# Kernel optimization log

Measured on AMD Instinct MI355X. Metric: run time of the kernel, lower is better.

The kernel has to match this reference:

```python
import jax, jax.numpy as jnp
import numpy as np

N_NODES = 50000
N_EDGES = 800000
IN_CH = 128
HID = 64
HEADS = 4
OUT_CH = 10
N_GRAPHS = 512
NEG_SLOPE = 0.2


def setup_inputs() -> dict:
    key = jax.random.key(0)
    ks = jax.random.split(key, 16)
    x = jax.random.normal(ks[0], (N_NODES, IN_CH), dtype=jnp.float32)
    edge_index = jax.random.randint(ks[1], (2, N_EDGES), 0, N_NODES, dtype=jnp.int64)
    batch = jnp.sort(jax.random.randint(ks[2], (N_NODES,), 0, N_GRAPHS, dtype=jnp.int64))
    s = 1.0 / np.sqrt(IN_CH)
    W1 = jax.random.uniform(ks[3], (IN_CH, HEADS * HID), jnp.float32, -s, s)
    att_src1 = jax.random.normal(ks[4], (HEADS, HID), jnp.float32) * 0.1
    att_dst1 = jax.random.normal(ks[5], (HEADS, HID), jnp.float32) * 0.1
    b1 = jnp.zeros((HEADS * HID,), jnp.float32)
    s2 = 1.0 / np.sqrt(HEADS * HID)
    W2 = jax.random.uniform(ks[6], (HEADS * HID, HID), jnp.float32, -s2, s2)
    att_src2 = jax.random.normal(ks[7], (1, HID), jnp.float32) * 0.1
    att_dst2 = jax.random.normal(ks[8], (1, HID), jnp.float32) * 0.1
    b2 = jnp.zeros((HID,), jnp.float32)
    s3 = 1.0 / np.sqrt(HID)
    Wl = jax.random.uniform(ks[9], (HID, OUT_CH), jnp.float32, -s3, s3)
    bl = jnp.zeros((OUT_CH,), jnp.float32)
    return dict(x=x, edge_index=edge_index, batch=batch,
                W1=W1, att_src1=att_src1, att_dst1=att_dst1, b1=b1,
                W2=W2, att_src2=att_src2, att_dst2=att_dst2, b2=b2,
                Wl=Wl, bl=bl)


def gat_conv(x, src, dst, W, att_src, att_dst, bias, heads, out_ch, concat):
    """PyG GATConv: gather -> per-edge attention -> segment softmax over dst -> scatter-add."""
    n = x.shape[0]
    h = (x @ W).reshape(n, heads, out_ch)            # [N,H,C]
    a_s = jnp.sum(h * att_src, axis=-1)              # [N,H]
    a_d = jnp.sum(h * att_dst, axis=-1)              # [N,H]
    e = jax.nn.leaky_relu(a_s[src] + a_d[dst], NEG_SLOPE)  # [E,H]
    m = jax.ops.segment_max(e, dst, num_segments=n)  # stable softmax per dst
    alpha = jnp.exp(e - m[dst])
    denom = jax.ops.segment_sum(alpha, dst, num_segments=n)
    alpha = alpha / denom[dst]
    out = jax.ops.segment_sum(h[src] * alpha[:, :, None], dst, num_segments=n)  # [N,H,C]
    if concat:
        out = out.reshape(n, heads * out_ch)
    else:
        out = out.mean(axis=1)
    return out + bias


def reference(x, edge_index, batch, W1, att_src1, att_dst1, b1,
              W2, att_src2, att_dst2, b2, Wl, bl):
    n = x.shape[0]
    # PyG GATConv default add_self_loops=True
    loops = jnp.arange(n, dtype=edge_index.dtype)
    src = jnp.concatenate([edge_index[0], loops])
    dst = jnp.concatenate([edge_index[1], loops])

    h = jax.nn.elu(gat_conv(x, src, dst, W1, att_src1, att_dst1, b1, HEADS, HID, True))
    h = jax.nn.elu(gat_conv(h, src, dst, W2, att_src2, att_dst2, b2, 1, HID, False))

    # global_mean_pool
    sums = jax.ops.segment_sum(h, batch, num_segments=N_GRAPHS)
    cnts = jax.ops.segment_sum(jnp.ones((n,), h.dtype), batch, num_segments=N_GRAPHS)
    pooled = sums / jnp.maximum(cnts, 1.0)[:, None]

    return pooled @ Wl + bl
```

## Files before the change

kernel.cpp:

```cpp
#include <hip/hip_runtime.h>
#include <hip/hip_bf16.h>
#include <math.h>

#define N_NODES 50000
#define N_EDGES 800000
#define IN_CH 128
#define HID 64
#define HEADS 4
#define OUT_CH 10
#define N_GRAPHS 512
#define NEG_SLOPE 0.2f

using short8_t = __attribute__((ext_vector_type(8))) short;
using f32x4 = __attribute__((ext_vector_type(4))) float;

__device__ __forceinline__ float b2f(unsigned short u) {
    return __uint_as_float(((unsigned)u) << 16);
}
__device__ __forceinline__ unsigned short f2b(float f) {
    __hip_bfloat16 b = __float2bfloat16(f);
    return *(unsigned short*)&b;
}
__device__ __forceinline__ short f2bs(float f) {
    __hip_bfloat16 b = __float2bfloat16(f);
    return *(short*)&b;
}
__device__ __forceinline__ float lrelu(float x) { return x > 0.f ? x : NEG_SLOPE * x; }

__global__ void convw_k(const float* __restrict__ W1, const float* __restrict__ W2,
                        unsigned short* __restrict__ Wt1, unsigned short* __restrict__ Wt2) {
    int idx = blockIdx.x * 256 + threadIdx.x;
    if (idx < 256 * 128) {
        int n = idx / 128, k = idx % 128;
        Wt1[idx] = f2b(W1[(size_t)k * 256 + n]);
    }
    int j = idx - 256 * 128;
    if (j >= 0 && j < 64 * 256) {
        int n = j / 256, k = j % 256;
        Wt2[j] = f2b(W2[(size_t)k * 64 + n]);
    }
}

__global__ __launch_bounds__(256) void mfma_gemm1_k(
        const float* __restrict__ X, const unsigned short* __restrict__ Wt,
        unsigned short* __restrict__ Yb,
        const float* __restrict__ asrc, const float* __restrict__ adst,
        float* __restrict__ As, float* __restrict__ Ad, int M) {
    const int lane = threadIdx.x & 63;
    const int w = threadIdx.x >> 6;
    const int r0 = blockIdx.x * 64 + w * 16;
    const int l15 = lane & 15;
    const int rc = min(r0 + l15, M - 1);
    const int kg = (lane >> 4) * 8;

    f32x4 acc[16] = {};
#pragma unroll
    for (int kc = 0; kc < 4; kc++) {
        int k0 = kc * 32 + kg;
        float4 xa = *(const float4*)&X[(size_t)rc * 128 + k0];
        float4 xb = *(const float4*)&X[(size_t)rc * 128 + k0 + 4];
        short8_t af;
        af[0] = f2bs(xa.x); af[1] = f2bs(xa.y); af[2] = f2bs(xa.z); af[3] = f2bs(xa.w);
        af[4] = f2bs(xb.x); af[5] = f2bs(xb.y); af[6] = f2bs(xb.z); af[7] = f2bs(xb.w);
#pragma unroll
        for (int ct = 0; ct < 16; ct++) {
            int col = ct * 16 + l15;
            short8_t bf = *(const short8_t*)&Wt[(size_t)col * 128 + k0];
            acc[ct] = __builtin_amdgcn_mfma_f32_16x16x32_bf16(af, bf, acc[ct], 0, 0, 0);
        }
    }

    const int rbase = r0 + (lane >> 4) * 4;
#pragma unroll
    for (int reg = 0; reg < 4; reg++) {
        int gr = rbase + reg;
        float s0 = 0.f, s1 = 0.f, s2 = 0.f, s3 = 0.f;
        float d0 = 0.f, d1 = 0.f, d2 = 0.f, d3 = 0.f;
#pragma unroll
        for (int cg = 0; cg < 4; cg++) {
            int c = cg * 16 + l15;
            float v0 = acc[0 * 4 + cg][reg], v1 = acc[1 * 4 + cg][reg];
            float v2 = acc[2 * 4 + cg][reg], v3 = acc[3 * 4 + cg][reg];
            s0 += v0 * asrc[0 * 64 + c]; d0 += v0 * adst[0 * 64 + c];
            s1 += v1 * asrc[1 * 64 + c]; d1 += v1 * adst[1 * 64 + c];
            s2 += v2 * asrc[2 * 64 + c]; d2 += v2 * adst[2 * 64 + c];
            s3 += v3 * asrc[3 * 64 + c]; d3 += v3 * adst[3 * 64 + c];
        }
#pragma unroll
        for (int o = 8; o > 0; o >>= 1) {
            s0 += __shfl_xor(s0, o); d0 += __shfl_xor(d0, o);
            s1 += __shfl_xor(s1, o); d1 += __shfl_xor(d1, o);
            s2 += __shfl_xor(s2, o); d2 += __shfl_xor(d2, o);
            s3 += __shfl_xor(s3, o); d3 += __shfl_xor(d3, o);
        }
        if (l15 == 0 && gr < M) {
            *(float4*)&As[gr * 4] = make_float4(s0, s1, s2, s3);
            *(float4*)&Ad[gr * 4] = make_float4(d0, d1, d2, d3);
        }
    }
#pragma unroll
    for (int reg = 0; reg < 4; reg++) {
        int gr = rbase + reg;
        if (gr >= M) continue;
#pragma unroll
        for (int cg = 0; cg < 4; cg++) {
            int c = cg * 16 + l15;
            ushort4 p;
            p.x = f2b(acc[0 * 4 + cg][reg]);
            p.y = f2b(acc[1 * 4 + cg][reg]);
            p.z = f2b(acc[2 * 4 + cg][reg]);
            p.w = f2b(acc[3 * 4 + cg][reg]);
            *(ushort4*)&Yb[(size_t)gr * 256 + c * 4] = p;
        }
    }
}

__global__ __launch_bounds__(256) void mfma_gemm2_k(
        const unsigned short* __restrict__ Xb, const unsigned short* __restrict__ Wt,
        unsigned short* __restrict__ Yb,
        const float* __restrict__ asrc, const float* __restrict__ adst,
        float* __restrict__ As, float* __restrict__ Ad, int M) {
    const int lane = threadIdx.x & 63;
    const int w = threadIdx.x >> 6;
    const int r0 = blockIdx.x * 64 + w * 16;
    const int l15 = lane & 15;
    const int rc = min(r0 + l15, M - 1);
    const int kg = (lane >> 4) * 8;

    f32x4 acc[4] = {};
#pragma unroll
    for (int kc = 0; kc < 8; kc++) {
        int k0 = kc * 32 + kg;
        short8_t af = *(const short8_t*)&Xb[(size_t)rc * 256 + k0];
#pragma unroll
        for (int ct = 0; ct < 4; ct++) {
            int col = ct * 16 + l15;
            short8_t bf = *(const short8_t*)&Wt[(size_t)col * 256 + k0];
            acc[ct] = __builtin_amdgcn_mfma_f32_16x16x32_bf16(af, bf, acc[ct], 0, 0, 0);
        }
    }

    const int rbase = r0 + (lane >> 4) * 4;
#pragma unroll
    for (int reg = 0; reg < 4; reg++) {
        int gr = rbase + reg;
        float sv = 0.f, dv = 0.f;
#pragma unroll
        for (int ct = 0; ct < 4; ct++) {
            int c = ct * 16 + l15;
            float v = acc[ct][reg];
            sv += v * asrc[c];
            dv += v * adst[c];
        }
#pragma unroll
        for (int o = 8; o > 0; o >>= 1) { sv += __shfl_xor(sv, o); dv += __shfl_xor(dv, o); }
        if (l15 == 0 && gr < M) { As[gr] = sv; Ad[gr] = dv; }
        if (gr < M) {
#pragma unroll
            for (int ct = 0; ct < 4; ct++)
                Yb[(size_t)gr * 64 + ct * 16 + l15] = f2b(acc[ct][reg]);
        }
    }
}

__global__ void hist_k(const int* __restrict__ dst, int* __restrict__ deg,
                       int* __restrict__ rank, int etot) {
    int nth = gridDim.x * 256;
    int i0 = blockIdx.x * 256 + threadIdx.x;
    int i1 = i0 + nth, i2 = i0 + 2 * nth, i3 = i0 + 3 * nth;
    bool v0 = i0 < etot, v1 = i1 < etot, v2 = i2 < etot, v3 = i3 < etot;
    int d0 = 0, d1 = 0, d2 = 0, d3 = 0;
    if (v0) d0 = (i0 < N_EDGES) ? dst[i0] : i0 - N_EDGES;
    if (v1) d1 = (i1 < N_EDGES) ? dst[i1] : i1 - N_EDGES;
    if (v2) d2 = (i2 < N_EDGES) ? dst[i2] : i2 - N_EDGES;
    if (v3) d3 = (i3 < N_EDGES) ? dst[i3] : i3 - N_EDGES;
    int r0 = 0, r1 = 0, r2 = 0, r3 = 0;
    if (v0) r0 = atomicAdd(&deg[d0], 1);
    if (v1) r1 = atomicAdd(&deg[d1], 1);
    if (v2) r2 = atomicAdd(&deg[d2], 1);
    if (v3) r3 = atomicAdd(&deg[d3], 1);
    if (v0) rank[i0] = r0;
    if (v1) rank[i1] = r1;
    if (v2) rank[i2] = r2;
    if (v3) rank[i3] = r3;
}

__global__ void cntg_k(const int* __restrict__ batch, float* __restrict__ cntf) {
    int g = blockIdx.x * 256 + threadIdx.x;
    if (g >= N_GRAPHS) return;
    int lo = 0, hi = N_NODES;
    while (lo < hi) { int mid = (lo + hi) >> 1; if (batch[mid] < g) lo = mid + 1; else hi = mid; }
    int lo2 = lo, hi2 = N_NODES;
    while (lo2 < hi2) { int mid = (lo2 + hi2) >> 1; if (batch[mid] < g + 1) lo2 = mid + 1; else hi2 = mid; }
    cntf[g] = (float)(lo2 - lo);
}

__global__ void blksum_k(const int* __restrict__ deg, int* __restrict__ bsum, int n) {
    int t = threadIdx.x;
    int i = blockIdx.x * 256 + t;
    int v = (i < n) ? deg[i] : 0;
#pragma unroll
    for (int o = 32; o > 0; o >>= 1) v += __shfl_xor(v, o);
    __shared__ int wsum[4];
    if ((t & 63) == 0) wsum[t >> 6] = v;
    __syncthreads();
    if (t == 0) bsum[blockIdx.x] = wsum[0] + wsum[1] + wsum[2] + wsum[3];
}

__global__ void scanb_k(int* __restrict__ bsum, int nb) {
    __shared__ int tmp[256];
    int t = threadIdx.x;
    int v = (t < nb) ? bsum[t] : 0;
    tmp[t] = v;
    __syncthreads();
    for (int o = 1; o < 256; o <<= 1) {
        int u = (t >= o) ? tmp[t - o] : 0;
        __syncthreads();
        tmp[t] += u;
        __syncthreads();
    }
    if (t < nb) bsum[t] = tmp[t] - v;
}

__global__ void scanapply_k(const int* __restrict__ deg, const int* __restrict__ bsum,
                            int* __restrict__ rowptr, int n) {
    __shared__ int tmp[256];
    int t = threadIdx.x;
    int i = blockIdx.x * 256 + t;
    int v = (i < n) ? deg[i] : 0;
    tmp[t] = v;
    __syncthreads();
    for (int o = 1; o < 256; o <<= 1) {
        int u = (t >= o) ? tmp[t - o] : 0;
        __syncthreads();
        tmp[t] += u;
        __syncthreads();
    }
    int boff = bsum[blockIdx.x];
    if (i < n) rowptr[i] = boff + tmp[t] - v;
    if (i == n - 1) rowptr[n] = boff + tmp[t];
}

__global__ void scatter_k(const int* __restrict__ src, const int* __restrict__ dst,
                          const int* __restrict__ rowptr, const int* __restrict__ rank,
                          int* __restrict__ csrc, int etot) {
    int i = blockIdx.x * blockDim.x + threadIdx.x;
    if (i >= etot) return;
    int s, d;
    if (i < N_EDGES) { s = src[i]; d = dst[i]; } else { s = d = i - N_EDGES; }
    csrc[rowptr[d] + rank[i]] = s;
}

__global__ void agg1_k(const int* __restrict__ rowptr, const int* __restrict__ csrc,
                       const float* __restrict__ As, const float* __restrict__ Ad,
                       const __hip_bfloat16* __restrict__ Hb,
                       const float* __restrict__ bias,
                       unsigned short* __restrict__ Outb, int nnodes) {
    __shared__ int ssh[4][64];
    __shared__ float4 wsh[4][64];
    int lane = threadIdx.x & 63;
    int w = threadIdx.x >> 6;
    int node = blockIdx.x * 4 + w;
    int beg = rowptr[node], end = rowptr[node + 1];
    int deg = end - beg;
    const unsigned short* hb = (const unsigned short*)Hb;
    float4 bv = *(const float4*)&Ad[node * 4];
    bool fast = (deg <= 64);
    if (fast) {
        bool act = lane < deg;
        int s = act ? csrc[beg + lane] : 0;
        float4 a = *(const float4*)&As[s * 4];
        float e0 = lrelu(a.x + bv.x), e1 = lrelu(a.y + bv.y);
        float e2 = lrelu(a.z + bv.z), e3 = lrelu(a.w + bv.w);
        if (!act) { e0 = e1 = e2 = e3 = -INFINITY; }
        float m0 = e0, m1 = e1, m2 = e2, m3 = e3;
#pragma unroll
        for (int o = 32; o > 0; o >>= 1) {
            m0 = fmaxf(m0, __shfl_xor(m0, o)); m1 = fmaxf(m1, __shfl_xor(m1, o));
            m2 = fmaxf(m2, __shfl_xor(m2, o)); m3 = fmaxf(m3, __shfl_xor(m3, o));
        }
        float x0 = act ? __expf(e0 - m0) : 0.f;
        float x1 = act ? __expf(e1 - m1) : 0.f;
        float x2 = act ? __expf(e2 - m2) : 0.f;
        float x3 = act ? __expf(e3 - m3) : 0.f;
        float d0 = x0, d1 = x1, d2 = x2, d3 = x3;
#pragma unroll
        for (int o = 32; o > 0; o >>= 1) {
            d0 += __shfl_xor(d0, o); d1 += __shfl_xor(d1, o);
            d2 += __shfl_xor(d2, o); d3 += __shfl_xor(d3, o);
        }
        ssh[w][lane] = s;
        wsh[w][lane] = make_float4(x0 / d0, x1 / d1, x2 / d2, x3 / d3);
    }
    __syncthreads();
    float acc0 = 0.f, acc1 = 0.f, acc2 = 0.f, acc3 = 0.f;
    if (fast) {
        float p0 = 0.f, p1 = 0.f, p2 = 0.f, p3 = 0.f;
        int j = 0;
        for (; j + 2 <= deg; j += 2) {
            int sA = ssh[w][j], sB = ssh[w][j + 1];
            float4 wA = wsh[w][j], wB = wsh[w][j + 1];
            ushort4 vA = *(const ushort4*)&hb[(size_t)sA * 256 + lane * 4];
            ushort4 vB = *(const ushort4*)&hb[(size_t)sB * 256 + lane * 4];
            acc0 += wA.x * b2f(vA.x); p0 += wB.x * b2f(vB.x);
            acc1 += wA.y * b2f(vA.y); p1 += wB.y * b2f(vB.y);
            acc2 += wA.z * b2f(vA.z); p2 += wB.z * b2f(vB.z);
            acc3 += wA.w * b2f(vA.w); p3 += wB.w * b2f(vB.w);
        }
        if (j < deg) {
            int s = ssh[w][j];
            float4 wt = wsh[w][j];
            ushort4 v = *(const ushort4*)&hb[(size_t)s * 256 + lane * 4];
            acc0 += wt.x * b2f(v.x); acc1 += wt.y * b2f(v.y);
            acc2 += wt.z * b2f(v.z); acc3 += wt.w * b2f(v.w);
        }
        acc0 += p0; acc1 += p1; acc2 += p2; acc3 += p3;
    } else {
        float m0 = -INFINITY, m1 = -INFINITY, m2 = -INFINITY, m3 = -INFINITY;
        for (int j = beg + lane; j < end; j += 64) {
            float4 a = *(const float4*)&As[csrc[j] * 4];
            m0 = fmaxf(m0, lrelu(a.x + bv.x)); m1 = fmaxf(m1, lrelu(a.y + bv.y));
            m2 = fmaxf(m2, lrelu(a.z + bv.z)); m3 = fmaxf(m3, lrelu(a.w + bv.w));
        }
#pragma unroll
        for (int o = 32; o > 0; o >>= 1) {
            m0 = fmaxf(m0, __shfl_xor(m0, o)); m1 = fmaxf(m1, __shfl_xor(m1, o));
            m2 = fmaxf(m2, __shfl_xor(m2, o)); m3 = fmaxf(m3, __shfl_xor(m3, o));
        }
        float d0 = 0.f, d1 = 0.f, d2 = 0.f, d3 = 0.f;
        for (int j = beg + lane; j < end; j += 64) {
            float4 a = *(const float4*)&As[csrc[j] * 4];
            d0 += __expf(lrelu(a.x + bv.x) - m0); d1 += __expf(lrelu(a.y + bv.y) - m1);
            d2 += __expf(lrelu(a.z + bv.z) - m2); d3 += __expf(lrelu(a.w + bv.w) - m3);
        }
#pragma unroll
        for (int o = 32; o > 0; o >>= 1) {
            d0 += __shfl_xor(d0, o); d1 += __shfl_xor(d1, o);
            d2 += __shfl_xor(d2, o); d3 += __shfl_xor(d3, o);
        }
        for (int j = beg; j < end; j++) {
            int s = csrc[j];
            float4 a = *(const float4*)&As[s * 4];
            float w0 = __expf(lrelu(a.x + bv.x) - m0) / d0;
            float w1 = __expf(lrelu(a.y + bv.y) - m1) / d1;
            float w2 = __expf(lrelu(a.z + bv.z) - m2) / d2;
            float w3 = __expf(lrelu(a.w + bv.w) - m3) / d3;
            ushort4 v = *(const ushort4*)&hb[(size_t)s * 256 + lane * 4];
            acc0 += w0 * b2f(v.x); acc1 += w1 * b2f(v.y);
            acc2 += w2 * b2f(v.z); acc3 += w3 * b2f(v.w);
        }
    }
    float r0 = acc0 + bias[0 * 64 + lane];
    float r1 = acc1 + bias[1 * 64 + lane];
    float r2 = acc2 + bias[2 * 64 + lane];
    float r3 = acc3 + bias[3 * 64 + lane];
    r0 = r0 > 0.f ? r0 : expm1f(r0);
    r1 = r1 > 0.f ? r1 : expm1f(r1);
    r2 = r2 > 0.f ? r2 : expm1f(r2);
    r3 = r3 > 0.f ? r3 : expm1f(r3);
    size_t base = (size_t)node * 256;
    Outb[base + 0 * 64 + lane] = f2b(r0);
    Outb[base + 1 * 64 + lane] = f2b(r1);
    Outb[base + 2 * 64 + lane] = f2b(r2);
    Outb[base + 3 * 64 + lane] = f2b(r3);
}

__global__ void agg2_k(const int* __restrict__ rowptr, const int* __restrict__ csrc,
                       const float* __restrict__ As, const float* __restrict__ Ad,
                       const __hip_bfloat16* __restrict__ Hb,
                       const float* __restrict__ bias, const int* __restrict__ batch,
                       float* __restrict__ pooled, int nnodes) {
    __shared__ int ssh[4][64];
    __shared__ float wsh[4][64];
    int lane = threadIdx.x & 63;
    int w = threadIdx.x >> 6;
    int node = blockIdx.x * 4 + w;
    int beg = rowptr[node], end = rowptr[node + 1];
    int deg = end - beg;
    const unsigned short* hb = (const unsigned short*)Hb;
    float ad = Ad[node];
    bool fast = (deg <= 64);
    if (fast) {
        bool act = lane < deg;
        int s = act ? csrc[beg + lane] : 0;
        float e = lrelu(As[s] + ad);
        if (!act) e = -INFINITY;
        float m = e;
#pragma unroll
        for (int o = 32; o > 0; o >>= 1) m = fmaxf(m, __shfl_xor(m, o));
        float x = act ? __expf(e - m) : 0.f;
        float d = x;
#pragma unroll
        for (int o = 32; o > 0; o >>= 1) d += __shfl_xor(d, o);
        ssh[w][lane] = s;
        wsh[w][lane] = x / d;
    }
    __syncthreads();
    float acc = 0.f;
    if (fast) {
        float p = 0.f;
        int j = 0;
        for (; j + 2 <= deg; j += 2) {
            int sA = ssh[w][j], sB = ssh[w][j + 1];
            float wA = wsh[w][j], wB = wsh[w][j + 1];
            acc += wA * b2f(hb[(size_t)sA * 64 + lane]);
            p   += wB * b2f(hb[(size_t)sB * 64 + lane]);
        }
        if (j < deg) acc += wsh[w][j] * b2f(hb[(size_t)ssh[w][j] * 64 + lane]);
        acc += p;
    } else {
        float m = -INFINITY;
        for (int j = beg + lane; j < end; j += 64) m = fmaxf(m, lrelu(As[csrc[j]] + ad));
#pragma unroll
        for (int o = 32; o > 0; o >>= 1) m = fmaxf(m, __shfl_xor(m, o));
        float d = 0.f;
        for (int j = beg + lane; j < end; j += 64) d += __expf(lrelu(As[csrc[j]] + ad) - m);
#pragma unroll
        for (int o = 32; o > 0; o >>= 1) d += __shfl_xor(d, o);
        for (int j = beg; j < end; j++) {
            int s = csrc[j];
            float wt = __expf(lrelu(As[s] + ad) - m) / d;
            acc += wt * b2f(hb[(size_t)s * 64 + lane]);
        }
    }
    float v = acc + bias[lane];
    v = v > 0.f ? v : expm1f(v);
    atomicAdd(&pooled[batch[node] * 64 + lane], v);
}

__global__ void final_k(const float* __restrict__ pooled, const float* __restrict__ cnt,
                        const float* __restrict__ Wl, const float* __restrict__ bl,
                        float* __restrict__ out) {
    int g = blockIdx.x;
    int t = threadIdx.x;
    __shared__ float s[64];
    float c = cnt[g];
    c = c > 1.f ? c : 1.f;
    s[t] = pooled[g * 64 + t] / c;
    __syncthreads();
    if (t < OUT_CH) {
        float acc = bl[t];
        for (int k = 0; k < 64; k++) acc += s[k] * Wl[k * OUT_CH + t];
        out[g * OUT_CH + t] = acc;
    }
}

extern "C" void kernel_launch(void* const* d_in, const int* in_sizes, int n_in,
                              void* d_out, int out_size, void* d_ws, size_t ws_size,
                              hipStream_t stream) {
    const float* x    = (const float*)d_in[0];
    const int*   ei   = (const int*)d_in[1];
    const int*   batch= (const int*)d_in[2];
    const float* W1   = (const float*)d_in[3];
    const float* as1  = (const float*)d_in[4];
    const float* ad1  = (const float*)d_in[5];
    const float* b1   = (const float*)d_in[6];
    const float* W2   = (const float*)d_in[7];
    const float* as2  = (const float*)d_in[8];
    const float* ad2  = (const float*)d_in[9];
    const float* b2   = (const float*)d_in[10];
    const float* Wl   = (const float*)d_in[11];
    const float* bl   = (const float*)d_in[12];
    float* out = (float*)d_out;

    const int* src = ei;
    const int* dst = ei + N_EDGES;
    const int ETOT = N_EDGES + N_NODES;
    const int NB = (N_NODES + 255) / 256;

    char* ws = (char*)d_ws;
    size_t off = 0;
    auto alloc = [&](size_t bytes) {
        void* p = ws + off;
        off = (off + bytes + 255) & ~((size_t)255);
        return p;
    };
    unsigned short* h1b  = (unsigned short*)alloc((size_t)N_NODES * 256 * 2);
    unsigned short* out1b= (unsigned short*)alloc((size_t)N_NODES * 256 * 2);
    float* As1    = (float*)alloc((size_t)N_NODES * 4 * 4);
    float* Ad1    = (float*)alloc((size_t)N_NODES * 4 * 4);
    float* As2    = (float*)alloc((size_t)N_NODES * 4);
    float* Ad2    = (float*)alloc((size_t)N_NODES * 4);
    int*   deg    = (int*)  alloc((size_t)N_NODES * 4);
    int*   rowptr = (int*)  alloc((size_t)(N_NODES + 1) * 4);
    int*   csrc   = (int*)  alloc((size_t)ETOT * 4);
    int*   rank   = (int*)  alloc((size_t)ETOT * 4);
    int*   bsum   = (int*)  alloc((size_t)NB * 4);
    unsigned short* Wt1 = (unsigned short*)alloc((size_t)256 * 128 * 2);
    unsigned short* Wt2 = (unsigned short*)alloc((size_t)64 * 256 * 2);
    float* pooled = (float*)alloc((size_t)N_GRAPHS * 64 * 4);
    float* cntf   = (float*)alloc((size_t)N_GRAPHS * 4);
    unsigned short* h2b = h1b;

    hipMemsetAsync(deg,    0, (size_t)N_NODES * 4, stream);
    hipMemsetAsync(pooled, 0, (size_t)N_GRAPHS * 64 * 4, stream);

    hist_k<<<(ETOT / 4 + 255) / 256, 256, 0, stream>>>(dst, deg, rank, ETOT);
    cntg_k<<<2, 256, 0, stream>>>(batch, cntf);
    blksum_k<<<NB, 256, 0, stream>>>(deg, bsum, N_NODES);
    scanb_k<<<1, 256, 0, stream>>>(bsum, NB);
    scanapply_k<<<NB, 256, 0, stream>>>(deg, bsum, rowptr, N_NODES);
    scatter_k<<<(ETOT + 255) / 256, 256, 0, stream>>>(src, dst, rowptr, rank, csrc, ETOT);
    convw_k<<<192, 256, 0, stream>>>(W1, W2, Wt1, Wt2);

    mfma_gemm1_k<<<(N_NODES + 63) / 64, 256, 0, stream>>>(x, Wt1, h1b, as1, ad1,
                                                          As1, Ad1, N_NODES);
    agg1_k<<<N_NODES / 4, 256, 0, stream>>>(rowptr, csrc, As1, Ad1,
                                            (const __hip_bfloat16*)h1b, b1, out1b, N_NODES);

    mfma_gemm2_k<<<(N_NODES + 63) / 64, 256, 0, stream>>>(out1b, Wt2, h2b, as2, ad2,
                                                          As2, Ad2, N_NODES);
    agg2_k<<<N_NODES / 4, 256, 0, stream>>>(rowptr, csrc, As2, Ad2,
                                            (const __hip_bfloat16*)h2b, b2, batch, pooled, N_NODES);

    final_k<<<N_GRAPHS, 64, 0, stream>>>(pooled, cntf, Wl, bl, out);
}
```

Measured before the change: 262.4 us.

## Fuse GEMM1, histogram, graph counts and pool zeroing into one launch; unroll gathers

```diff
diff --git a/kernel.cpp b/kernel.cpp
--- a/kernel.cpp
+++ b/kernel.cpp
@@ -11,6 +11,11 @@
 #define N_GRAPHS 512
 #define NEG_SLOPE 0.2f
 
+#define ETOT_C (N_EDGES + N_NODES)
+#define GB1 ((N_NODES + 63) / 64)
+#define GH  ((ETOT_C / 4 + 255) / 256)
+#define GZ  32
+
 using short8_t = __attribute__((ext_vector_type(8))) short;
 using f32x4 = __attribute__((ext_vector_type(4))) float;
 
@@ -41,78 +46,121 @@
     }
 }
 
-__global__ __launch_bounds__(256) void mfma_gemm1_k(
+__global__ __launch_bounds__(256) void mega1_k(
         const float* __restrict__ X, const unsigned short* __restrict__ Wt,
         unsigned short* __restrict__ Yb,
         const float* __restrict__ asrc, const float* __restrict__ adst,
-        float* __restrict__ As, float* __restrict__ Ad, int M) {
-    const int lane = threadIdx.x & 63;
-    const int w = threadIdx.x >> 6;
-    const int r0 = blockIdx.x * 64 + w * 16;
-    const int l15 = lane & 15;
-    const int rc = min(r0 + l15, M - 1);
-    const int kg = (lane >> 4) * 8;
-
-    f32x4 acc[16] = {};
-#pragma unroll
-    for (int kc = 0; kc < 4; kc++) {
-        int k0 = kc * 32 + kg;
-        float4 xa = *(const float4*)&X[(size_t)rc * 128 + k0];
-        float4 xb = *(const float4*)&X[(size_t)rc * 128 + k0 + 4];
-        short8_t af;
-        af[0] = f2bs(xa.x); af[1] = f2bs(xa.y); af[2] = f2bs(xa.z); af[3] = f2bs(xa.w);
-        af[4] = f2bs(xb.x); af[5] = f2bs(xb.y); af[6] = f2bs(xb.z); af[7] = f2bs(xb.w);
-#pragma unroll
-        for (int ct = 0; ct < 16; ct++) {
-            int col = ct * 16 + l15;
-            short8_t bf = *(const short8_t*)&Wt[(size_t)col * 128 + k0];
-            acc[ct] = __builtin_amdgcn_mfma_f32_16x16x32_bf16(af, bf, acc[ct], 0, 0, 0);
-        }
-    }
-
-    const int rbase = r0 + (lane >> 4) * 4;
-#pragma unroll
-    for (int reg = 0; reg < 4; reg++) {
-        int gr = rbase + reg;
-        float s0 = 0.f, s1 = 0.f, s2 = 0.f, s3 = 0.f;
-        float d0 = 0.f, d1 = 0.f, d2 = 0.f, d3 = 0.f;
-#pragma unroll
-        for (int cg = 0; cg < 4; cg++) {
-            int c = cg * 16 + l15;
-            float v0 = acc[0 * 4 + cg][reg], v1 = acc[1 * 4 + cg][reg];
-            float v2 = acc[2 * 4 + cg][reg], v3 = acc[3 * 4 + cg][reg];
-            s0 += v0 * asrc[0 * 64 + c]; d0 += v0 * adst[0 * 64 + c];
-            s1 += v1 * asrc[1 * 64 + c]; d1 += v1 * adst[1 * 64 + c];
-            s2 += v2 * asrc[2 * 64 + c]; d2 += v2 * adst[2 * 64 + c];
-            s3 += v3 * asrc[3 * 64 + c]; d3 += v3 * adst[3 * 64 + c];
-        }
-#pragma unroll
-        for (int o = 8; o > 0; o >>= 1) {
-            s0 += __shfl_xor(s0, o); d0 += __shfl_xor(d0, o);
-            s1 += __shfl_xor(s1, o); d1 += __shfl_xor(d1, o);
-            s2 += __shfl_xor(s2, o); d2 += __shfl_xor(d2, o);
-            s3 += __shfl_xor(s3, o); d3 += __shfl_xor(d3, o);
-        }
-        if (l15 == 0 && gr < M) {
-            *(float4*)&As[gr * 4] = make_float4(s0, s1, s2, s3);
-            *(float4*)&Ad[gr * 4] = make_float4(d0, d1, d2, d3);
-        }
-    }
-#pragma unroll
-    for (int reg = 0; reg < 4; reg++) {
-        int gr = rbase + reg;
-        if (gr >= M) continue;
-#pragma unroll
-        for (int cg = 0; cg < 4; cg++) {
-            int c = cg * 16 + l15;
-            ushort4 p;
-            p.x = f2b(acc[0 * 4 + cg][reg]);
-            p.y = f2b(acc[1 * 4 + cg][reg]);
-            p.z = f2b(acc[2 * 4 + cg][reg]);
-            p.w = f2b(acc[3 * 4 + cg][reg]);
-            *(ushort4*)&Yb[(size_t)gr * 256 + c * 4] = p;
-        }
-    }
+        float* __restrict__ As, float* __restrict__ Ad, int M,
+        const int* __restrict__ dst, int* __restrict__ deg, int* __restrict__ rank,
+        const int* __restrict__ batch, float* __restrict__ cntf,
+        float* __restrict__ pooled) {
+    int b = blockIdx.x;
+    if (b < GB1) {
+        const int lane = threadIdx.x & 63;
+        const int w = threadIdx.x >> 6;
+        const int r0 = b * 64 + w * 16;
+        const int l15 = lane & 15;
+        const int rc = min(r0 + l15, M - 1);
+        const int kg = (lane >> 4) * 8;
+
+        f32x4 acc[16] = {};
+#pragma unroll
+        for (int kc = 0; kc < 4; kc++) {
+            int k0 = kc * 32 + kg;
+            float4 xa = *(const float4*)&X[(size_t)rc * 128 + k0];
+            float4 xb = *(const float4*)&X[(size_t)rc * 128 + k0 + 4];
+            short8_t af;
+            af[0] = f2bs(xa.x); af[1] = f2bs(xa.y); af[2] = f2bs(xa.z); af[3] = f2bs(xa.w);
+            af[4] = f2bs(xb.x); af[5] = f2bs(xb.y); af[6] = f2bs(xb.z); af[7] = f2bs(xb.w);
+#pragma unroll
+            for (int ct = 0; ct < 16; ct++) {
+                int col = ct * 16 + l15;
+                short8_t bf = *(const short8_t*)&Wt[(size_t)col * 128 + k0];
+                acc[ct] = __builtin_amdgcn_mfma_f32_16x16x32_bf16(af, bf, acc[ct], 0, 0, 0);
+            }
+        }
+
+        const int rbase = r0 + (lane >> 4) * 4;
+#pragma unroll
+        for (int reg = 0; reg < 4; reg++) {
+            int gr = rbase + reg;
+            float s0 = 0.f, s1 = 0.f, s2 = 0.f, s3 = 0.f;
+            float d0 = 0.f, d1 = 0.f, d2 = 0.f, d3 = 0.f;
+#pragma unroll
+            for (int cg = 0; cg < 4; cg++) {
+                int c = cg * 16 + l15;
+                float v0 = acc[0 * 4 + cg][reg], v1 = acc[1 * 4 + cg][reg];
+                float v2 = acc[2 * 4 + cg][reg], v3 = acc[3 * 4 + cg][reg];
+                s0 += v0 * asrc[0 * 64 + c]; d0 += v0 * adst[0 * 64 + c];
+                s1 += v1 * asrc[1 * 64 + c]; d1 += v1 * adst[1 * 64 + c];
+                s2 += v2 * asrc[2 * 64 + c]; d2 += v2 * adst[2 * 64 + c];
+                s3 += v3 * asrc[3 * 64 + c]; d3 += v3 * adst[3 * 64 + c];
+            }
+#pragma unroll
+            for (int o = 8; o > 0; o >>= 1) {
+                s0 += __shfl_xor(s0, o); d0 += __shfl_xor(d0, o);
+                s1 += __shfl_xor(s1, o); d1 += __shfl_xor(d1, o);
+                s2 += __shfl_xor(s2, o); d2 += __shfl_xor(d2, o);
+                s3 += __shfl_xor(s3, o); d3 += __shfl_xor(d3, o);
+            }
+            if (l15 == 0 && gr < M) {
+                *(float4*)&As[gr * 4] = make_float4(s0, s1, s2, s3);
+                *(float4*)&Ad[gr * 4] = make_float4(d0, d1, d2, d3);
+            }
+        }
+#pragma unroll
+        for (int reg = 0; reg < 4; reg++) {
+            int gr = rbase + reg;
+            if (gr >= M) continue;
+#pragma unroll
+            for (int cg = 0; cg < 4; cg++) {
+                int c = cg * 16 + l15;
+                ushort4 p;
+                p.x = f2b(acc[0 * 4 + cg][reg]);
+                p.y = f2b(acc[1 * 4 + cg][reg]);
+                p.z = f2b(acc[2 * 4 + cg][reg]);
+                p.w = f2b(acc[3 * 4 + cg][reg]);
+                *(ushort4*)&Yb[(size_t)gr * 256 + c * 4] = p;
+            }
+        }
+        return;
+    }
+    b -= GB1;
+    if (b < GH) {
+        const int nth = GH * 256;
+        int i0 = b * 256 + threadIdx.x;
+        int i1 = i0 + nth, i2 = i0 + 2 * nth, i3 = i0 + 3 * nth;
+        bool v0 = i0 < ETOT_C, v1 = i1 < ETOT_C, v2 = i2 < ETOT_C, v3 = i3 < ETOT_C;
+        int d0 = 0, d1 = 0, d2 = 0, d3 = 0;
+        if (v0) d0 = (i0 < N_EDGES) ? dst[i0] : i0 - N_EDGES;
+        if (v1) d1 = (i1 < N_EDGES) ? dst[i1] : i1 - N_EDGES;
+        if (v2) d2 = (i2 < N_EDGES) ? dst[i2] : i2 - N_EDGES;
+        if (v3) d3 = (i3 < N_EDGES) ? dst[i3] : i3 - N_EDGES;
+        int r0 = 0, r1 = 0, r2 = 0, r3 = 0;
+        if (v0) r0 = atomicAdd(&deg[d0], 1);
+        if (v1) r1 = atomicAdd(&deg[d1], 1);
+        if (v2) r2 = atomicAdd(&deg[d2], 1);
+        if (v3) r3 = atomicAdd(&deg[d3], 1);
+        if (v0) rank[i0] = r0;
+        if (v1) rank[i1] = r1;
+        if (v2) rank[i2] = r2;
+        if (v3) rank[i3] = r3;
+        return;
+    }
+    b -= GH;
+    if (b < 2) {
+        int g = b * 256 + threadIdx.x;
+        if (g >= N_GRAPHS) return;
+        int lo = 0, hi = N_NODES;
+        while (lo < hi) { int mid = (lo + hi) >> 1; if (batch[mid] < g) lo = mid + 1; else hi = mid; }
+        int lo2 = lo, hi2 = N_NODES;
+        while (lo2 < hi2) { int mid = (lo2 + hi2) >> 1; if (batch[mid] < g + 1) lo2 = mid + 1; else hi2 = mid; }
+        cntf[g] = (float)(lo2 - lo);
+        return;
+    }
+    b -= 2;
+    int idx = b * 256 + threadIdx.x;
+    *(float4*)&pooled[(size_t)idx * 4] = make_float4(0.f, 0.f, 0.f, 0.f);
 }
 
 __global__ __launch_bounds__(256) void mfma_gemm2_k(
@@ -161,38 +209,6 @@
                 Yb[(size_t)gr * 64 + ct * 16 + l15] = f2b(acc[ct][reg]);
         }
     }
-}
-
-__global__ void hist_k(const int* __restrict__ dst, int* __restrict__ deg,
-                       int* __restrict__ rank, int etot) {
-    int nth = gridDim.x * 256;
-    int i0 = blockIdx.x * 256 + threadIdx.x;
-    int i1 = i0 + nth, i2 = i0 + 2 * nth, i3 = i0 + 3 * nth;
-    bool v0 = i0 < etot, v1 = i1 < etot, v2 = i2 < etot, v3 = i3 < etot;
-    int d0 = 0, d1 = 0, d2 = 0, d3 = 0;
-    if (v0) d0 = (i0 < N_EDGES) ? dst[i0] : i0 - N_EDGES;
-    if (v1) d1 = (i1 < N_EDGES) ? dst[i1] : i1 - N_EDGES;
-    if (v2) d2 = (i2 < N_EDGES) ? dst[i2] : i2 - N_EDGES;
-    if (v3) d3 = (i3 < N_EDGES) ? dst[i3] : i3 - N_EDGES;
-    int r0 = 0, r1 = 0, r2 = 0, r3 = 0;
-    if (v0) r0 = atomicAdd(&deg[d0], 1);
-    if (v1) r1 = atomicAdd(&deg[d1], 1);
-    if (v2) r2 = atomicAdd(&deg[d2], 1);
-    if (v3) r3 = atomicAdd(&deg[d3], 1);
-    if (v0) rank[i0] = r0;
-    if (v1) rank[i1] = r1;
-    if (v2) rank[i2] = r2;
-    if (v3) rank[i3] = r3;
-}
-
-__global__ void cntg_k(const int* __restrict__ batch, float* __restrict__ cntf) {
-    int g = blockIdx.x * 256 + threadIdx.x;
-    if (g >= N_GRAPHS) return;
-    int lo = 0, hi = N_NODES;
-    while (lo < hi) { int mid = (lo + hi) >> 1; if (batch[mid] < g) lo = mid + 1; else hi = mid; }
-    int lo2 = lo, hi2 = N_NODES;
-    while (lo2 < hi2) { int mid = (lo2 + hi2) >> 1; if (batch[mid] < g + 1) lo2 = mid + 1; else hi2 = mid; }
-    cntf[g] = (float)(lo2 - lo);
 }
 
 __global__ void blksum_k(const int* __restrict__ deg, int* __restrict__ bsum, int n) {
@@ -297,17 +313,23 @@
     if (fast) {
         float p0 = 0.f, p1 = 0.f, p2 = 0.f, p3 = 0.f;
         int j = 0;
-        for (; j + 2 <= deg; j += 2) {
-            int sA = ssh[w][j], sB = ssh[w][j + 1];
-            float4 wA = wsh[w][j], wB = wsh[w][j + 1];
+        for (; j + 4 <= deg; j += 4) {
+            int sA = ssh[w][j], sB = ssh[w][j + 1], sC = ssh[w][j + 2], sD = ssh[w][j + 3];
+            float4 wA = wsh[w][j], wB = wsh[w][j + 1], wC = wsh[w][j + 2], wD = wsh[w][j + 3];
             ushort4 vA = *(const ushort4*)&hb[(size_t)sA * 256 + lane * 4];
             ushort4 vB = *(const ushort4*)&hb[(size_t)sB * 256 + lane * 4];
-            acc0 += wA.x * b2f(vA.x); p0 += wB.x * b2f(vB.x);
-            acc1 += wA.y * b2f(vA.y); p1 += wB.y * b2f(vB.y);
-            acc2 += wA.z * b2f(vA.z); p2 += wB.z * b2f(vB.z);
-            acc3 += wA.w * b2f(vA.w); p3 += wB.w * b2f(vB.w);
-        }
-        if (j < deg) {
+            ushort4 vC = *(const ushort4*)&hb[(size_t)sC * 256 + lane * 4];
+            ushort4 vD = *(const ushort4*)&hb[(size_t)sD * 256 + lane * 4];
+            acc0 += wA.x * b2f(vA.x) + wC.x * b2f(vC.x);
+            p0   += wB.x * b2f(vB.x) + wD.x * b2f(vD.x);
+            acc1 += wA.y * b2f(vA.y) + wC.y * b2f(vC.y);
+            p1   += wB.y * b2f(vB.y) + wD.y * b2f(vD.y);
+            acc2 += wA.z * b2f(vA.z) + wC.z * b2f(vC.z);
+            p2   += wB.z * b2f(vB.z) + wD.z * b2f(vD.z);
+            acc3 += wA.w * b2f(vA.w) + wC.w * b2f(vC.w);
+            p3   += wB.w * b2f(vB.w) + wD.w * b2f(vD.w);
+        }
+        for (; j < deg; j++) {
             int s = ssh[w][j];
             float4 wt = wsh[w][j];
             ushort4 v = *(const ushort4*)&hb[(size_t)s * 256 + lane * 4];
@@ -400,13 +422,13 @@
     if (fast) {
         float p = 0.f;
         int j = 0;
-        for (; j + 2 <= deg; j += 2) {
-            int sA = ssh[w][j], sB = ssh[w][j + 1];
-            float wA = wsh[w][j], wB = wsh[w][j + 1];
-            acc += wA * b2f(hb[(size_t)sA * 64 + lane]);
-            p   += wB * b2f(hb[(size_t)sB * 64 + lane]);
-        }
-        if (j < deg) acc += wsh[w][j] * b2f(hb[(size_t)ssh[w][j] * 64 + lane]);
+        for (; j + 4 <= deg; j += 4) {
+            int sA = ssh[w][j], sB = ssh[w][j + 1], sC = ssh[w][j + 2], sD = ssh[w][j + 3];
+            float wA = wsh[w][j], wB = wsh[w][j + 1], wC = wsh[w][j + 2], wD = wsh[w][j + 3];
+            acc += wA * b2f(hb[(size_t)sA * 64 + lane]) + wC * b2f(hb[(size_t)sC * 64 + lane]);
+            p   += wB * b2f(hb[(size_t)sB * 64 + lane]) + wD * b2f(hb[(size_t)sD * 64 + lane]);
+        }
+        for (; j < deg; j++) acc += wsh[w][j] * b2f(hb[(size_t)ssh[w][j] * 64 + lane]);
         acc += p;
     } else {
         float m = -INFINITY;
@@ -465,7 +487,7 @@
 
     const int* src = ei;
     const int* dst = ei + N_EDGES;
-    const int ETOT = N_EDGES + N_NODES;
+    const int ETOT = ETOT_C;
     const int NB = (N_NODES + 255) / 256;
 
     char* ws = (char*)d_ws;
@@ -492,19 +514,18 @@
     float* cntf   = (float*)alloc((size_t)N_GRAPHS * 4);
     unsigned short* h2b = h1b;
 
-    hipMemsetAsync(deg,    0, (size_t)N_NODES * 4, stream);
-    hipMemsetAsync(pooled, 0, (size_t)N_GRAPHS * 64 * 4, stream);
-
-    hist_k<<<(ETOT / 4 + 255) / 256, 256, 0, stream>>>(dst, deg, rank, ETOT);
-    cntg_k<<<2, 256, 0, stream>>>(batch, cntf);
+    hipMemsetAsync(deg, 0, (size_t)N_NODES * 4, stream);
+
+    convw_k<<<192, 256, 0, stream>>>(W1, W2, Wt1, Wt2);
+    mega1_k<<<GB1 + GH + 2 + GZ, 256, 0, stream>>>(
+        x, Wt1, h1b, as1, ad1, As1, Ad1, N_NODES,
+        dst, deg, rank, batch, cntf, pooled);
+
     blksum_k<<<NB, 256, 0, stream>>>(deg, bsum, N_NODES);
     scanb_k<<<1, 256, 0, stream>>>(bsum, NB);
     scanapply_k<<<NB, 256, 0, stream>>>(deg, bsum, rowptr, N_NODES);
     scatter_k<<<(ETOT + 255) / 256, 256, 0, stream>>>(src, dst, rowptr, rank, csrc, ETOT);
-    convw_k<<<192, 256, 0, stream>>>(W1, W2, Wt1, Wt2);
-
-    mfma_gemm1_k<<<(N_NODES + 63) / 64, 256, 0, stream>>>(x, Wt1, h1b, as1, ad1,
-                                                          As1, Ad1, N_NODES);
+
     agg1_k<<<N_NODES / 4, 256, 0, stream>>>(rowptr, csrc, As1, Ad1,
                                             (const __hip_bfloat16*)h1b, b1, out1b, N_NODES);
 
```

Result: faster. 234.6 us (-10.6%).
